# Kernel tuning notes

Measured on AMD Instinct MI355X. Metric: run time of the kernel, lower is better.

Reference implementation:

```python
import jax, jax.numpy as jnp
import numpy as np
import math

L_SIDE = 32           # one_side_length = ceil(sqrt(L)), L = 32**2
NDIM = 16             # args.ndim (SSM state size)
N_SSM = 16            # args.n_ssm
DIRS = 4              # args.directions_amount
EMBED = 1024          # embed_dim
KD = DIRS * N_SSM     # kernel_dim = 64
CDIM = EMBED * DIRS   # C_dimensions = 4096
H = EMBED // N_SSM    # 64 (channels per ssm)
R2 = 16               # expansion terms per kernel position
R = L_SIDE * L_SIDE * R2
V = 2 * L_SIDE        # vander power dim (power_dim = kernel_dim_arg*2)
BSZ = 8
SEQ = L_SIDE * L_SIDE


def _build_one_matrix():
    # Mimics CoeffCalculator.whole_as_one: for each of d=2 flow axes and each
    # of R expansion terms, the 4 A-factor rows are one-hot selectors over the
    # V power basis, and the 5th (B) row holds an integer coefficient in one of
    # the first two columns (selecting B1 or B2).
    rng = np.random.default_rng(0)
    M = np.zeros((2, 5, R, V), dtype=np.float32)
    di = np.arange(2)[:, None]
    ri = np.arange(R)[None, :]
    for a in range(4):
        idx = rng.integers(0, V, size=(2, R))
        M[di, a, ri, idx] = 1.0
    col = rng.integers(0, 2, size=(2, R))
    coef = rng.integers(1, 5, size=(2, R)).astype(np.float32)
    M[di, 4, ri, col] = coef
    return jnp.asarray(M)


def setup_inputs() -> dict:
    key = jax.random.key(0)
    ks = jax.random.split(key, 7)
    return {
        "x": jax.random.normal(ks[0], (SEQ, BSZ, EMBED), jnp.float32),
        "A": jax.random.normal(ks[1], (4, KD, NDIM), jnp.float32) * 0.2,
        "B1": jax.random.normal(ks[2], (KD, NDIM), jnp.float32) * 0.2,
        "B2": jax.random.normal(ks[3], (KD, NDIM), jnp.float32) * 0.2,
        "C1": jax.random.normal(ks[4], (CDIM, NDIM), jnp.float32),
        "C2": jax.random.normal(ks[5], (CDIM, NDIM), jnp.float32),
        "omega": jax.random.normal(ks[6], (EMBED,), jnp.float32),
        "one_matrix": _build_one_matrix(),
    }


def _compute_kernel(A, B1, B2, C1, C2, one_matrix, dtype):
    scale = 1.0 / math.sqrt(NDIM)
    # _calc_coeffs: sigmoid on A, B
    As = jax.nn.sigmoid(A)                                  # (4, KD, NDIM)
    pw = jnp.arange(V, dtype=dtype)
    # torch.linalg.vander: increasing powers 0..V-1 -> (4, V, KD, NDIM)
    A_vals = jnp.transpose(As[..., None] ** pw, (0, 3, 1, 2))
    Bs = jax.nn.sigmoid(jnp.stack([B1, B2], 0))             # (2, KD, NDIM)
    Bpad = jnp.zeros((V, KD, NDIM), dtype).at[:2].set(Bs)   # pad to V rows
    vals = jnp.concatenate([A_vals, Bpad[None]], 0)         # (5, V, KD, NDIM)
    # 'd a R V, a V k n -> d a R k n' then product over the 5 factors
    prod = jnp.einsum('drv,vkn->drkn', one_matrix[:, 0], vals[0])
    for a in range(1, 5):
        prod = prod * jnp.einsum('drv,vkn->drkn', one_matrix[:, a], vals[a])
    # sum over r2 expansion terms per kernel position
    w = prod.reshape(2, SEQ, R2, KD, NDIM).sum(2)           # (2, SEQ, KD, NDIM)
    C = jnp.stack([C1, C2], 0) * scale                      # (2, CDIM, NDIM)
    Cr = C.reshape(2, H, KD, NDIM)
    k = jnp.einsum('dpkn,dhkn->phk', w, Cr).reshape(L_SIDE, L_SIDE, CDIM)
    # boundary scaling (first row/col x2, corner net x1)
    k = k.at[0, :, :].multiply(2.0)
    k = k.at[:, 0, :].multiply(2.0)
    k = k.at[0, 0, :].divide(4.0)
    return k


def reference(x, A, B1, B2, C1, C2, omega, one_matrix):
    k = _compute_kernel(A, B1, B2, C1, C2, one_matrix, x.dtype)
    # channel layout (H, dir, n_ssm) -> per-direction (EMBED,) kernels
    kd = k.reshape(L_SIDE, L_SIDE, H, DIRS, N_SSM)
    kd = jnp.transpose(kd, (3, 2, 4, 0, 1)).reshape(DIRS, EMBED, L_SIDE, L_SIDE)
    # 4-corner scans: flip kernel per direction; conv is linear so sum kernels
    ksum = kd[0] + kd[1, :, ::-1, :] + kd[2, :, :, ::-1] + kd[3, :, ::-1, ::-1]
    residual = x * omega                                    # 'L B D, D -> L B D'
    xg = jnp.transpose(x, (1, 2, 0)).reshape(BSZ, EMBED, L_SIDE, L_SIDE)
    s = 2 * L_SIDE
    xf = jnp.fft.rfft2(xg, s=(s, s))                        # (B, D, s, s//2+1)
    kf = jnp.fft.rfft2(ksum, s=(s, s))
    y = jnp.fft.irfft2(xf * kf, s=(s, s))[..., :L_SIDE, :L_SIDE]
    y = jnp.transpose(y.reshape(BSZ, EMBED, SEQ), (2, 0, 1))  # back to (L, B, D)
    return y + residual
```

## Files before the change

kernel.cpp:

```cpp
#include <hip/hip_runtime.h>
#include <stdint.h>


typedef __attribute__((ext_vector_type(8))) short short8;
typedef __attribute__((ext_vector_type(4))) float f32x4;

__device__ inline uint16_t f2bf(float f) {
    uint32_t u = __float_as_uint(f);
    uint32_t r = (u + 0x7FFFu + ((u >> 16) & 1u)) >> 16;
    return (uint16_t)r;
}
__device__ inline float bf2f(uint16_t v) {
    return __uint_as_float((uint32_t)v << 16);
}
__device__ inline uint32_t packbf(float a, float b) {
    return (uint32_t)f2bf(a) | ((uint32_t)f2bf(b) << 16);
}

__global__ __launch_bounds__(256) void k_pre(const float* __restrict__ x,
                                             uint16_t* __restrict__ xtb,
                                             const float* __restrict__ om,
                                             const float* __restrict__ A,
                                             const float* __restrict__ B1,
                                             const float* __restrict__ B2,
                                             uint32_t* __restrict__ selg,
                                             float* __restrict__ coefg,
                                             float* __restrict__ LAg,
                                             float* __restrict__ SBg) {
    __shared__ __align__(16) float shf[32 * 257];
    int bx = blockIdx.x;
    int t = threadIdx.x;

    if (bx < 2048 && (bx & 1) == 0) {
        int bi = bx >> 1;
        int u = bi & 31, e0 = (bi >> 5) * 32;
        {
            int c = t & 7, a = t >> 3;
            const float* src = x + (size_t)(u * 256) * 1024 + e0 + c * 4;
            #pragma unroll
            for (int qq = 0; qq < 8; ++qq) {
                int r = qq * 32 + a;
                float4 v = *(const float4*)(src + (size_t)r * 1024);
                shf[(c * 4 + 0) * 257 + r] = v.x;
                shf[(c * 4 + 1) * 257 + r] = v.y;
                shf[(c * 4 + 2) * 257 + r] = v.z;
                shf[(c * 4 + 3) * 257 + r] = v.w;
            }
        }
        __syncthreads();
        {
            int e_local = t >> 3, c = t & 7;
            const float* row = shf + e_local * 257;
            uint16_t* dst = xtb + (size_t)(e0 + e_local) * 8192 + u * 256;
            #pragma unroll
            for (int qq = 0; qq < 4; ++qq) {
                int b = qq * 2 + (c >> 2);
                int v0 = (c & 3) * 8;
                uint32_t pk0 = packbf(row[(v0 + 0) * 8 + b], row[(v0 + 1) * 8 + b]);
                uint32_t pk1 = packbf(row[(v0 + 2) * 8 + b], row[(v0 + 3) * 8 + b]);
                uint32_t pk2 = packbf(row[(v0 + 4) * 8 + b], row[(v0 + 5) * 8 + b]);
                uint32_t pk3 = packbf(row[(v0 + 6) * 8 + b], row[(v0 + 7) * 8 + b]);
                *(uint4*)(dst + b * 32 + v0) = make_uint4(pk0, pk1, pk2, pk3);
            }
        }
    } else if (bx < 2048) {
        int p = bx >> 1;
        int lane = t & 63, wv = t >> 6;
        #pragma unroll
        for (int k = 0; k < 8; ++k) {
            int pi = wv * 8 + k;
            int d = pi >> 4, r2 = pi & 15;
            int r = p * 16 + r2;
            const float* rb = om + ((size_t)d * 5242880 + (size_t)r * 64);
            uint32_t s = 0;
            #pragma unroll
            for (int a = 0; a < 4; ++a) {
                float v = rb[(size_t)a * 1048576 + lane];
                unsigned long long m = __ballot(v != 0.0f);
                uint32_t idx = ((uint32_t)__builtin_ctzll(m)) & 63u;
                s |= idx << (6 * a);
            }
            if (lane == 0) {
                float r0 = rb[4 * 1048576 + 0];
                float r1 = rb[4 * 1048576 + 1];
                uint32_t col = (r1 != 0.0f) ? 1u : 0u;
                selg[d * 16384 + r] = s | (col << 24);
                coefg[d * 16384 + r] = r0 + r1;
            }
        }
    } else {
        int i = bx - 2048;
        int e = t * 4;
        if (i < 4) {
            float4 v = *(const float4*)(A + i * 1024 + e);
            float4 o;
            o.x = -log2f(1.0f + expf(-v.x));
            o.y = -log2f(1.0f + expf(-v.y));
            o.z = -log2f(1.0f + expf(-v.z));
            o.w = -log2f(1.0f + expf(-v.w));
            *(float4*)(LAg + i * 1024 + e) = o;
        } else {
            const float* Bs = (i == 4) ? B1 : B2;
            float4 v = *(const float4*)(Bs + e);
            float4 o;
            o.x = 1.0f / (1.0f + expf(-v.x));
            o.y = 1.0f / (1.0f + expf(-v.y));
            o.z = 1.0f / (1.0f + expf(-v.z));
            o.w = 1.0f / (1.0f + expf(-v.w));
            *(float4*)(SBg + (i - 4) * 1024 + e) = o;
        }
    }
}

__global__ __launch_bounds__(256) void k_w(const uint32_t* __restrict__ selg,
                                           const float* __restrict__ coefg,
                                           const float* __restrict__ LAg,
                                           const float* __restrict__ SBg,
                                           float* __restrict__ w) {
    __shared__ uint32_t sel_l[32];
    __shared__ float coef_l[32];
    int p = blockIdx.x;
    int t = threadIdx.x;
    if (t < 32) {
        int d = t >> 4, r2 = t & 15;
        sel_l[t]  = selg[d * 16384 + p * 16 + r2];
        coef_l[t] = coefg[d * 16384 + p * 16 + r2];
    }
    __syncthreads();

    int d = t >> 7;
    int j0 = (t & 127) * 8;
    float L0[8], L1[8], L2[8], L3[8], B0v[8], B1v[8], acc[8];
    #pragma unroll
    for (int a = 0; a < 4; ++a) {
        float* La = (a == 0) ? L0 : (a == 1) ? L1 : (a == 2) ? L2 : L3;
        float4 u0 = *(const float4*)(LAg + a * 1024 + j0);
        float4 u1 = *(const float4*)(LAg + a * 1024 + j0 + 4);
        La[0] = u0.x; La[1] = u0.y; La[2] = u0.z; La[3] = u0.w;
        La[4] = u1.x; La[5] = u1.y; La[6] = u1.z; La[7] = u1.w;
    }
    {
        float4 u0 = *(const float4*)(SBg + j0);
        float4 u1 = *(const float4*)(SBg + j0 + 4);
        float4 v0 = *(const float4*)(SBg + 1024 + j0);
        float4 v1 = *(const float4*)(SBg + 1024 + j0 + 4);
        B0v[0] = u0.x; B0v[1] = u0.y; B0v[2] = u0.z; B0v[3] = u0.w;
        B0v[4] = u1.x; B0v[5] = u1.y; B0v[6] = u1.z; B0v[7] = u1.w;
        B1v[0] = v0.x; B1v[1] = v0.y; B1v[2] = v0.z; B1v[3] = v0.w;
        B1v[4] = v1.x; B1v[5] = v1.y; B1v[6] = v1.z; B1v[7] = v1.w;
    }
    #pragma unroll
    for (int jj = 0; jj < 8; ++jj) acc[jj] = 0.0f;

    #pragma unroll
    for (int r2 = 0; r2 < 16; ++r2) {
        uint32_t s = sel_l[d * 16 + r2];
        float cf = coef_l[d * 16 + r2];
        float f0 = (float)(s & 63u);
        float f1 = (float)((s >> 6) & 63u);
        float f2 = (float)((s >> 12) & 63u);
        float f3 = (float)((s >> 18) & 63u);
        int col = (int)((s >> 24) & 1u);
        float c0 = col ? 0.0f : cf;
        float c1 = col ? cf : 0.0f;
        #pragma unroll
        for (int jj = 0; jj < 8; ++jj) {
            float ex = __builtin_fmaf(f3, L3[jj],
                       __builtin_fmaf(f2, L2[jj],
                       __builtin_fmaf(f1, L1[jj], f0 * L0[jj])));
            float bs = __builtin_fmaf(c1, B1v[jj], c0 * B0v[jj]);
            acc[jj] = __builtin_fmaf(exp2f(ex), bs, acc[jj]);
        }
    }
    float* dst = w + (size_t)(d * 1024 + p) * 1024 + j0;
    *(float4*)(dst)     = make_float4(acc[0], acc[1], acc[2], acc[3]);
    *(float4*)(dst + 4) = make_float4(acc[4], acc[5], acc[6], acc[7]);
}

__global__ __launch_bounds__(256) void k_kd(const float* __restrict__ w,
                                            const float* __restrict__ C1,
                                            const float* __restrict__ C2,
                                            uint16_t* __restrict__ kd4b) {
    __shared__ float Wl[128 * 33];
    __shared__ float Ctl[32 * 65];
    int kap = blockIdx.x;
    int p0 = blockIdx.y * 128;
    int dir = kap >> 4, m = kap & 15;
    int t = threadIdx.x;

    {
        int off = (t & 3) * 4;
        #pragma unroll
        for (int rep = 0; rep < 4; ++rep) {
            int row_id = rep * 64 + (t >> 2);
            int d = row_id >> 7, pp = row_id & 127;
            const float* src = w + ((size_t)(d * 1024 + p0 + pp) * 64 + kap) * 16 + off;
            float4 v = *(const float4*)src;
            float* dstl = Wl + pp * 33 + d * 16 + off;
            dstl[0] = v.x; dstl[1] = v.y; dstl[2] = v.z; dstl[3] = v.w;
        }
    }
    if (t < 128) {
        int d = t >> 6, h = t & 63;
        const float* Cd = d ? C2 : C1;
        const float* src = Cd + (size_t)(h * 64 + kap) * 16;
        #pragma unroll
        for (int q = 0; q < 16; ++q)
            Ctl[(d * 16 + q) * 65 + h] = src[q] * 0.25f;
    }
    __syncthreads();

    int ph = t & 15, hq = t >> 4;
    int pl = ph * 8, h0 = hq * 4;
    float acc[8][4];
    #pragma unroll
    for (int i = 0; i < 8; ++i)
        { acc[i][0] = acc[i][1] = acc[i][2] = acc[i][3] = 0.0f; }

    for (int k = 0; k < 32; ++k) {
        float c0 = Ctl[k * 65 + h0 + 0];
        float c1 = Ctl[k * 65 + h0 + 1];
        float c2 = Ctl[k * 65 + h0 + 2];
        float c3 = Ctl[k * 65 + h0 + 3];
        #pragma unroll
        for (int i = 0; i < 8; ++i) {
            float wv = Wl[(pl + i) * 33 + k];
            acc[i][0] += wv * c0; acc[i][1] += wv * c1;
            acc[i][2] += wv * c2; acc[i][3] += wv * c3;
        }
    }
    #pragma unroll
    for (int j = 0; j < 4; ++j) {
        int h = h0 + j;
        uint32_t pk[4];
        #pragma unroll
        for (int qq = 0; qq < 4; ++qq) {
            float v0, v1;
            #pragma unroll
            for (int z = 0; z < 2; ++z) {
                int p = p0 + pl + qq * 2 + z;
                int ii = p >> 5, jj = p & 31;
                float f = ((ii == 0) != (jj == 0)) ? 2.0f : 1.0f;
                float val = acc[qq * 2 + z][j] * f;
                if (z == 0) v0 = val; else v1 = val;
            }
            pk[qq] = packbf(v0, v1);
        }
        uint16_t* dst = kd4b + ((size_t)(dir * 1024 + h * 16 + m)) * 1024 + p0 + pl;
        *(uint4*)dst = make_uint4(pk[0], pk[1], pk[2], pk[3]);
    }
}

__global__ __launch_bounds__(256) void k_conv(const uint16_t* __restrict__ xtb,
                                              const uint16_t* __restrict__ kd4b,
                                              uint16_t* __restrict__ ytb) {
    __shared__ __align__(16) char smem[24576 + 16384];
    const int KROW = 768;
    const int SROW = 96;
    char* xtl = smem + 24576;

    int e = blockIdx.x;
    int t = threadIdx.x;
    int lane = t & 63, wv = t >> 6;
    int n = lane & 15, q = lane >> 4, nn = n & 7;

    {
        f32x4 z = {0.f, 0.f, 0.f, 0.f};
        #pragma unroll
        for (int k = 0; k < 6; ++k)
            *(f32x4*)(smem + (t + k * 256) * 16) = z;
    }
    {
        const uint4* src = (const uint4*)(xtb + (size_t)e * 8192);
        #pragma unroll
        for (int r = 0; r < 4; ++r) {
            uint4 v = src[r * 256 + t];
            *(uint4*)(xtl + (r * 256 + t) * 16) = v;
        }
    }
    int pi = t >> 3, pj = (t & 7) * 4;
    float s0, s1, s2, s3;
    {
        const uint16_t* b0 = kd4b + (size_t)e * 1024;
        ushort4 a0 = *(const ushort4*)(b0 + pi * 32 + pj);
        ushort4 a1 = *(const ushort4*)(b0 + (1 << 20) + (31 - pi) * 32 + pj);
        ushort4 a2 = *(const ushort4*)(b0 + (2 << 20) + pi * 32 + (28 - pj));
        ushort4 a3 = *(const ushort4*)(b0 + (3 << 20) + (31 - pi) * 32 + (28 - pj));
        s0 = bf2f(a0.x) + bf2f(a1.x) + bf2f(a2.w) + bf2f(a3.w);
        s1 = bf2f(a0.y) + bf2f(a1.y) + bf2f(a2.z) + bf2f(a3.z);
        s2 = bf2f(a0.z) + bf2f(a1.z) + bf2f(a2.y) + bf2f(a3.y);
        s3 = bf2f(a0.w) + bf2f(a1.w) + bf2f(a2.x) + bf2f(a3.x);
    }
    __syncthreads();

    {
        uint16_t k0 = f2bf(s0), k1 = f2bf(s1), k2 = f2bf(s2), k3 = f2bf(s3);
        #pragma unroll
        for (int s = 0; s < 8; ++s) {
            uint16_t* row = (uint16_t*)(smem + pi * KROW + s * SROW);
            int c = 31 + s - pj;
            row[c]     = k0;
            row[c - 1] = k1;
            row[c - 2] = k2;
            row[c - 3] = k3;
        }
    }
    __syncthreads();

    int A0 = n - 8 * q;
    int A1 = A0 + 16;
    int sh1 = (A1 + 9) & 7;
    int off1 = sh1 * SROW + (31 + sh1 - A1) * 2;
    int off0;
    if (A0 >= -8) {
        int sh0 = (A0 + 9) & 7;
        off0 = sh0 * SROW + (31 + sh0 - A0) * 2;
    } else {
        off0 = 80;
    }
    int boff = nn * 64 + q * 16;

    short8 Breg[16];
    #pragma unroll
    for (int u = 0; u < 16; ++u)
        Breg[u] = *(const short8*)(xtl + u * 512 + boff);

    f32x4 acc0[8], acc1[8];
    #pragma unroll
    for (int ii = 0; ii < 8; ++ii) {
        acc0[ii] = (f32x4){0.f, 0.f, 0.f, 0.f};
        acc1[ii] = (f32x4){0.f, 0.f, 0.f, 0.f};
    }

    #pragma unroll
    for (int dd = 0; dd < 4; ++dd) {
        if (dd <= wv) {
            const char* krow = smem + (wv - dd) * KROW;
            short8 a0 = *(const short8*)(krow + off0);
            short8 a1 = *(const short8*)(krow + off1);
            #pragma unroll
            for (int ii = 0; ii < 8; ++ii) {
                short8 bb = (ii < 4) ? Breg[dd + 4 * ii]
                                     : *(const short8*)(xtl + (dd + 4 * ii) * 512 + boff);
                acc0[ii] = __builtin_amdgcn_mfma_f32_16x16x32_bf16(a0, bb, acc0[ii], 0, 0, 0);
                acc1[ii] = __builtin_amdgcn_mfma_f32_16x16x32_bf16(a1, bb, acc1[ii], 0, 0, 0);
            }
        }
    }
    #pragma unroll
    for (int g = 1; g <= 7; ++g) {
        #pragma unroll
        for (int dd = 0; dd < 4; ++dd) {
            const char* krow = smem + (wv + 4 * g - 3 + dd) * KROW;
            short8 a0 = *(const short8*)(krow + off0);
            short8 a1 = *(const short8*)(krow + off1);
            #pragma unroll
            for (int ii = g; ii < 8; ++ii) {
                int u = 4 * (ii - g) + 3 - dd;
                short8 bb = (ii - g < 4) ? Breg[u]
                                         : *(const short8*)(xtl + u * 512 + boff);
                acc0[ii] = __builtin_amdgcn_mfma_f32_16x16x32_bf16(a0, bb, acc0[ii], 0, 0, 0);
                acc1[ii] = __builtin_amdgcn_mfma_f32_16x16x32_bf16(a1, bb, acc1[ii], 0, 0, 0);
            }
        }
    }

    if (n < 8) {
        uint16_t* base = ytb + ((size_t)(n * 1024 + e)) * 1024 + q * 4;
        #pragma unroll
        for (int ii = 0; ii < 8; ++ii) {
            int i = wv + 4 * ii;
            uint2 w0 = make_uint2(packbf(acc0[ii][0], acc0[ii][1]),
                                  packbf(acc0[ii][2], acc0[ii][3]));
            uint2 w1 = make_uint2(packbf(acc1[ii][0], acc1[ii][1]),
                                  packbf(acc1[ii][2], acc1[ii][3]));
            *(uint2*)(base + i * 32)      = w0;
            *(uint2*)(base + i * 32 + 16) = w1;
        }
    }
}

__global__ __launch_bounds__(256) void k_t2(const uint16_t* __restrict__ ytb,
                                            const float* __restrict__ x,
                                            const float* __restrict__ omega,
                                            float* __restrict__ out) {
    __shared__ float lds[32 * 130];
    int e0 = blockIdx.x * 32, p0 = blockIdx.y * 128, b = blockIdx.z;
    int t = threadIdx.x;
    {
        int a = t >> 3, c = t & 7;
        const uint16_t* src = ytb + (size_t)(b * 1024 + e0 + a) * 1024 + p0;
        float* dst = lds + a * 130;
        #pragma unroll
        for (int rep = 0; rep < 2; ++rep) {
            int off = (c + rep * 8) * 8;
            uint4 v = *(const uint4*)(src + off);
            uint32_t ww[4] = {v.x, v.y, v.z, v.w};
            #pragma unroll
            for (int k = 0; k < 4; ++k) {
                float2 f;
                f.x = bf2f((uint16_t)(ww[k] & 0xFFFFu));
                f.y = bf2f((uint16_t)(ww[k] >> 16));
                *(float2*)(dst + off + k * 2) = f;
            }
        }
    }
    __syncthreads();
    int pl = t >> 1, eh = (t & 1) * 16;
    int p = p0 + pl;
    const float* xs = x + ((size_t)(p * 8 + b)) * 1024 + e0 + eh;
    float* os = out + ((size_t)(p * 8 + b)) * 1024 + e0 + eh;
    #pragma unroll
    for (int qq = 0; qq < 4; ++qq) {
        float4 xv = *(const float4*)(xs + qq * 4);
        int eb = eh + qq * 4;
        float4 ov;
        ov.x = lds[(eb + 0) * 130 + pl] + xv.x * omega[e0 + eb + 0];
        ov.y = lds[(eb + 1) * 130 + pl] + xv.y * omega[e0 + eb + 1];
        ov.z = lds[(eb + 2) * 130 + pl] + xv.z * omega[e0 + eb + 2];
        ov.w = lds[(eb + 3) * 130 + pl] + xv.w * omega[e0 + eb + 3];
        *(float4*)(os + qq * 4) = ov;
    }
}

extern "C" void kernel_launch(void* const* d_in, const int* in_sizes, int n_in,
                              void* d_out, int out_size, void* d_ws, size_t ws_size,
                              hipStream_t stream) {
    (void)in_sizes; (void)n_in; (void)out_size; (void)ws_size;
    const float* x   = (const float*)d_in[0];
    const float* A   = (const float*)d_in[1];
    const float* B1  = (const float*)d_in[2];
    const float* B2  = (const float*)d_in[3];
    const float* C1  = (const float*)d_in[4];
    const float* C2  = (const float*)d_in[5];
    const float* omg = (const float*)d_in[6];
    const float* om  = (const float*)d_in[7];
    float* out = (float*)d_out;

    float* ws  = (float*)d_ws;
    uint16_t* xtb  = (uint16_t*)ws;
    uint16_t* kd4b = (uint16_t*)(ws + 4194304);
    uint16_t* ytb  = (uint16_t*)(ws + 6291456);
    float* w       = ws + 10485760;
    uint32_t* selg = (uint32_t*)(ws + 4194304);
    float* coefg   = ws + 4194304 + 32768;
    float* LAg     = ws + 4194304 + 65536;
    float* SBg     = ws + 4194304 + 69632;

    k_pre <<<2054, 256, 0, stream>>>(x, xtb, om, A, B1, B2, selg, coefg, LAg, SBg);
    k_w   <<<1024, 256, 0, stream>>>(selg, coefg, LAg, SBg, w);
    k_kd  <<<dim3(64, 8), 256, 0, stream>>>(w, C1, C2, kd4b);
    k_conv<<<1024, 256, 0, stream>>>(xtb, kd4b, ytb);
    k_t2  <<<dim3(32, 8, 8), 256, 0, stream>>>(ytb, x, omg, out);
}
```

Baseline: 194.8 us.

## Fuse one_matrix selector decoding into k_w via dot-product index extraction

Moves decoding of the one-hot one_matrix rows out of k_pre and into k_w, removing the selg/coefg intermediate buffers and their global round trip. Each row's selected index is now recovered as a dot product of the row with 0..63 instead of ballot/ctz, and the B coefficients are read straight from the matrix. k_pre shrinks to the transpose and sigmoid blocks. k_w now reads the one_matrix rows itself with coalesced float4 loads, so the 4-factor selection generalises slightly differently: it only holds when each A row is exactly one-hot.

After: 189.9 us. -2.5%, faster.

```diff
diff --git a/kernel.cpp b/kernel.cpp
--- a/kernel.cpp
+++ b/kernel.cpp
@@ -19,21 +19,17 @@
 
 __global__ __launch_bounds__(256) void k_pre(const float* __restrict__ x,
                                              uint16_t* __restrict__ xtb,
-                                             const float* __restrict__ om,
                                              const float* __restrict__ A,
                                              const float* __restrict__ B1,
                                              const float* __restrict__ B2,
-                                             uint32_t* __restrict__ selg,
-                                             float* __restrict__ coefg,
                                              float* __restrict__ LAg,
                                              float* __restrict__ SBg) {
     __shared__ __align__(16) float shf[32 * 257];
     int bx = blockIdx.x;
     int t = threadIdx.x;
 
-    if (bx < 2048 && (bx & 1) == 0) {
-        int bi = bx >> 1;
-        int u = bi & 31, e0 = (bi >> 5) * 32;
+    if (bx < 1024) {
+        int u = bx & 31, e0 = (bx >> 5) * 32;
         {
             int c = t & 7, a = t >> 3;
             const float* src = x + (size_t)(u * 256) * 1024 + e0 + c * 4;
@@ -63,33 +59,8 @@
                 *(uint4*)(dst + b * 32 + v0) = make_uint4(pk0, pk1, pk2, pk3);
             }
         }
-    } else if (bx < 2048) {
-        int p = bx >> 1;
-        int lane = t & 63, wv = t >> 6;
-        #pragma unroll
-        for (int k = 0; k < 8; ++k) {
-            int pi = wv * 8 + k;
-            int d = pi >> 4, r2 = pi & 15;
-            int r = p * 16 + r2;
-            const float* rb = om + ((size_t)d * 5242880 + (size_t)r * 64);
-            uint32_t s = 0;
-            #pragma unroll
-            for (int a = 0; a < 4; ++a) {
-                float v = rb[(size_t)a * 1048576 + lane];
-                unsigned long long m = __ballot(v != 0.0f);
-                uint32_t idx = ((uint32_t)__builtin_ctzll(m)) & 63u;
-                s |= idx << (6 * a);
-            }
-            if (lane == 0) {
-                float r0 = rb[4 * 1048576 + 0];
-                float r1 = rb[4 * 1048576 + 1];
-                uint32_t col = (r1 != 0.0f) ? 1u : 0u;
-                selg[d * 16384 + r] = s | (col << 24);
-                coefg[d * 16384 + r] = r0 + r1;
-            }
-        }
     } else {
-        int i = bx - 2048;
+        int i = bx - 1024;
         int e = t * 4;
         if (i < 4) {
             float4 v = *(const float4*)(A + i * 1024 + e);
@@ -112,19 +83,36 @@
     }
 }
 
-__global__ __launch_bounds__(256) void k_w(const uint32_t* __restrict__ selg,
-                                           const float* __restrict__ coefg,
+__global__ __launch_bounds__(256) void k_w(const float* __restrict__ om,
                                            const float* __restrict__ LAg,
                                            const float* __restrict__ SBg,
                                            float* __restrict__ w) {
-    __shared__ uint32_t sel_l[32];
-    __shared__ float coef_l[32];
+    __shared__ float ff[2][16][4];
+    __shared__ float cf[2][16][2];
     int p = blockIdx.x;
     int t = threadIdx.x;
-    if (t < 32) {
-        int d = t >> 4, r2 = t & 15;
-        sel_l[t]  = selg[d * 16384 + p * 16 + r2];
-        coef_l[t] = coefg[d * 16384 + p * 16 + r2];
+    {
+        int row_id = t >> 1, h = t & 1;
+        int d = row_id >> 6, a = (row_id >> 4) & 3, r2 = row_id & 15;
+        const float* src = om + ((size_t)(d * 5 + a) * 16384 + p * 16 + r2) * 64 + h * 32;
+        float s = 0.0f;
+        #pragma unroll
+        for (int q = 0; q < 8; ++q) {
+            float4 v = *(const float4*)(src + q * 4);
+            float jb = (float)(h * 32 + q * 4);
+            s = __builtin_fmaf(v.x, jb,
+                __builtin_fmaf(v.y, jb + 1.0f,
+                __builtin_fmaf(v.z, jb + 2.0f,
+                __builtin_fmaf(v.w, jb + 3.0f, s))));
+        }
+        s += __shfl_xor(s, 1);
+        if (h == 0) ff[d][r2][a] = s;
+        if (t < 32) {
+            int dd = t >> 4, rr = t & 15;
+            const float* c = om + ((size_t)(dd * 5 + 4) * 16384 + p * 16 + rr) * 64;
+            cf[dd][rr][0] = c[0];
+            cf[dd][rr][1] = c[1];
+        }
     }
     __syncthreads();
 
@@ -154,15 +142,12 @@
 
     #pragma unroll
     for (int r2 = 0; r2 < 16; ++r2) {
-        uint32_t s = sel_l[d * 16 + r2];
-        float cf = coef_l[d * 16 + r2];
-        float f0 = (float)(s & 63u);
-        float f1 = (float)((s >> 6) & 63u);
-        float f2 = (float)((s >> 12) & 63u);
-        float f3 = (float)((s >> 18) & 63u);
-        int col = (int)((s >> 24) & 1u);
-        float c0 = col ? 0.0f : cf;
-        float c1 = col ? cf : 0.0f;
+        float f0 = ff[d][r2][0];
+        float f1 = ff[d][r2][1];
+        float f2 = ff[d][r2][2];
+        float f3 = ff[d][r2][3];
+        float c0 = cf[d][r2][0];
+        float c1 = cf[d][r2][1];
         #pragma unroll
         for (int jj = 0; jj < 8; ++jj) {
             float ex = __builtin_fmaf(f3, L3[jj],
@@ -442,13 +427,11 @@
     uint16_t* kd4b = (uint16_t*)(ws + 4194304);
     uint16_t* ytb  = (uint16_t*)(ws + 6291456);
     float* w       = ws + 10485760;
-    uint32_t* selg = (uint32_t*)(ws + 4194304);
-    float* coefg   = ws + 4194304 + 32768;
     float* LAg     = ws + 4194304 + 65536;
     float* SBg     = ws + 4194304 + 69632;
 
-    k_pre <<<2054, 256, 0, stream>>>(x, xtb, om, A, B1, B2, selg, coefg, LAg, SBg);
-    k_w   <<<1024, 256, 0, stream>>>(selg, coefg, LAg, SBg, w);
+    k_pre <<<1030, 256, 0, stream>>>(x, xtb, A, B1, B2, LAg, SBg);
+    k_w   <<<1024, 256, 0, stream>>>(om, LAg, SBg, w);
     k_kd  <<<dim3(64, 8), 256, 0, stream>>>(w, C1, C2, kd4b);
     k_conv<<<1024, 256, 0, stream>>>(xtb, kd4b, ytb);
     k_t2  <<<dim3(32, 8, 8), 256, 0, stream>>>(ytb, x, omg, out);
```
